# Kernel tuning notes

Hardware: AMD Instinct MI355X
Metric: run time of the kernel (lower is better)

Reference implementation:

```python
import jax, jax.numpy as jnp
import numpy as np

N_NODES = 30000
N_EDGES = 480000
NFEAT = 256
HEADS = 4
C0 = 64      # layer0 out_channels
C1 = 40      # layer1 out_channels = nclass
NEG_SLOPE = 0.2
EPS = 1e-16


def glorot(key, shape, fan):
    # PyG glorot: uniform(-s, s), s = sqrt(6/(fan_in+fan_out)) over last 2 dims
    s = float(np.sqrt(6.0 / fan))
    return jax.random.uniform(key, shape, jnp.float32, -s, s)


def setup_inputs() -> dict:
    key = jax.random.key(0)
    ks = jax.random.split(key, 10)
    x = jax.random.normal(ks[0], (N_NODES, NFEAT), jnp.float32)
    src = jax.random.randint(ks[1], (N_EDGES,), 0, N_NODES)
    off = jax.random.randint(ks[2], (N_EDGES,), 1, N_NODES)
    dst = (src + off) % N_NODES  # guaranteed no self loops
    edge_index = jnp.stack([src, dst]).astype(jnp.int64)
    # layer 0 params (in=256 -> heads*out = 4*64, concat=True)
    w0 = glorot(ks[3], (NFEAT, HEADS * C0), NFEAT + HEADS * C0)
    att0 = glorot(ks[4], (1, HEADS, 2 * C0), HEADS + 2 * C0)
    b0 = jnp.zeros((HEADS * C0,), jnp.float32)
    # layer 1 params (in=256 -> heads*out = 4*40, concat=False)
    w1 = glorot(ks[5], (HEADS * C0, HEADS * C1), HEADS * C0 + HEADS * C1)
    att1 = glorot(ks[6], (1, HEADS, 2 * C1), HEADS + 2 * C1)
    b1 = jnp.zeros((C1,), jnp.float32)
    return {"x": x, "edge_index": edge_index, "w0": w0, "att0": att0,
            "b0": b0, "w1": w1, "att1": att1, "b1": b1}


def geo_layer(x, row, col, W, att, bias, heads, out_ch, concat):
    n = x.shape[0]
    h = (x @ W).reshape(n, heads, out_ch)          # [N,H,C]
    x_i = h[row]                                   # [E,H,C] gather (target per old-PyG i=0)
    x_j = h[col]                                   # [E,H,C]
    # 'gat' attention: leaky_relu(sum(cat(x_i,x_j) * att))
    a_l = att[:, :, :out_ch]
    a_r = att[:, :, out_ch:]
    alpha = jnp.sum(x_i * a_l, -1) + jnp.sum(x_j * a_r, -1)   # [E,H]
    alpha = jax.nn.leaky_relu(alpha, NEG_SLOPE)
    # segment softmax over target node (row)
    amax = jax.ops.segment_max(alpha, row, num_segments=n)
    ex = jnp.exp(alpha - amax[row])
    denom = jax.ops.segment_sum(ex, row, num_segments=n)
    alpha = ex / (denom[row] + EPS)
    neighbor = x_j * alpha[..., None]              # [E,H,C]
    out = jax.ops.segment_sum(neighbor, row, num_segments=n)  # [N,H,C]
    if concat:
        out = out.reshape(n, heads * out_ch)
    else:
        out = out.mean(axis=1)
    return out + bias


def reference(x, edge_index, w0, att0, b0, w1, att1, b1):
    n = x.shape[0]
    loops = jnp.arange(n, dtype=edge_index.dtype)
    row = jnp.concatenate([edge_index[0], loops])
    col = jnp.concatenate([edge_index[1], loops])
    out = geo_layer(x, row, col, w0, att0, b0, HEADS, C0, True)
    out = jax.nn.relu(out)
    out = geo_layer(out, row, col, w1, att1, b1, HEADS, C1, False)
    return out  # [N, nclass]
```

## Files before the change

kernel.cpp:

```cpp
#include <hip/hip_runtime.h>
#include <math.h>

#define N_NODES 30000
#define N_EDGESN 480000
#define NFEAT 256
#define HEADS 4
#define C0V 64
#define C1V 40
#define HC0 (HEADS*C0V)
#define HC1 (HEADS*C1V)
#define NEG_SLOPE 0.2f
#define EPSV 1e-16f
#define KDIM 256
#define KPAD 264

typedef unsigned short ushort_t;
typedef __attribute__((ext_vector_type(8))) short short8v;
typedef __attribute__((ext_vector_type(4))) float f32x4;

__device__ __forceinline__ float lrelu(float x) { return x >= 0.f ? x : x * NEG_SLOPE; }

__device__ __forceinline__ float b2f_lo(unsigned int u) {
  union { unsigned int u; float f; } v; v.u = u << 16; return v.f;
}
__device__ __forceinline__ float b2f_hi(unsigned int u) {
  union { unsigned int u; float f; } v; v.u = u & 0xffff0000u; return v.f;
}
__device__ __forceinline__ unsigned short f2b(float f) {
  union { float f; unsigned int u; } v; v.f = f;
  unsigned int u = v.u + 0x7FFFu + ((v.u >> 16) & 1u);
  return (unsigned short)(u >> 16);
}

__global__ __launch_bounds__(256) void prep_kernel(const float* __restrict__ W0,
    const float* __restrict__ W1, ushort_t* __restrict__ W0t,
    ushort_t* __restrict__ W1t, int* __restrict__ zp, int zn) {
  const int idx = blockIdx.x * 256 + threadIdx.x;
  constexpr int T0 = NFEAT * HC0;
  constexpr int T1 = HC0 * HC1;
  if (idx < T0) {
    const int k = idx / HC0, nf = idx - k * HC0;
    W0t[(size_t)nf * NFEAT + k] = f2b(W0[idx]);
  } else if (idx < T0 + T1) {
    const int i2 = idx - T0;
    const int k = i2 / HC1, nf = i2 - k * HC1;
    W1t[(size_t)nf * HC0 + k] = f2b(W1[i2]);
  }
  if (idx < zn) zp[idx] = 0;
}

template <int NFW, int CG, bool A_F32, int FUSE, int NT>
__global__ __launch_bounds__(NT) void gemm_mfma3(const void* __restrict__ Ap,
    const ushort_t* __restrict__ Wt, ushort_t* __restrict__ C, int nblk,
    const float* __restrict__ att, float* __restrict__ al, float* __restrict__ ar) {
  constexpr int S = N_NODES / 16;
  constexpr int N = CG * NFW * 16;
  constexpr int NCH = 16 * (KDIM / 8) / NT;
  __shared__ ushort_t As[2][16][KPAD];
  const int tid = threadIdx.x;
  const int lane = tid & 63, cg = tid >> 6;
  const int r_a = lane & 15, kg = lane >> 4;

  short8v B[8][NFW];
#pragma unroll
  for (int ks = 0; ks < 8; ++ks)
#pragma unroll
    for (int f = 0; f < NFW; ++f)
      B[ks][f] = *reinterpret_cast<const short8v*>(
          Wt + (size_t)((cg * NFW + f) * 16 + r_a) * KDIM + ks * 32 + kg * 8);

#define STAGE_LOAD(STRIP, STG)                                                   \
  _Pragma("unroll")                                                              \
  for (int q = 0; q < NCH; ++q) {                                                \
    const int c = tid + q * NT;                                                  \
    const int r = c >> 5, ko = (c & 31) * 8;                                     \
    if (A_F32) {                                                                 \
      const float* A = (const float*)Ap + (size_t)((STRIP) * 16 + r) * KDIM + ko;\
      const float4 lo = *reinterpret_cast<const float4*>(A);                     \
      const float4 hi = *reinterpret_cast<const float4*>(A + 4);                 \
      STG[q].x = (unsigned)f2b(lo.x) | ((unsigned)f2b(lo.y) << 16);              \
      STG[q].y = (unsigned)f2b(lo.z) | ((unsigned)f2b(lo.w) << 16);              \
      STG[q].z = (unsigned)f2b(hi.x) | ((unsigned)f2b(hi.y) << 16);              \
      STG[q].w = (unsigned)f2b(hi.z) | ((unsigned)f2b(hi.w) << 16);              \
    } else {                                                                     \
      STG[q] = *reinterpret_cast<const uint4*>(                                  \
          (const ushort_t*)Ap + (size_t)((STRIP) * 16 + r) * KDIM + ko);         \
    }                                                                            \
  }
#define STAGE_WRITE(BUF, STG)                                                    \
  _Pragma("unroll")                                                              \
  for (int q = 0; q < NCH; ++q) {                                                \
    const int c = tid + q * NT;                                                  \
    const int r = c >> 5, ko = (c & 31) * 8;                                     \
    *reinterpret_cast<uint4*>(&As[BUF][r][ko]) = STG[q];                         \
  }

  int strip = blockIdx.x;
  {
    uint4 stg[NCH];
    STAGE_LOAD(strip, stg)
    STAGE_WRITE(0, stg)
  }
  __syncthreads();

  int buf = 0;
  while (true) {
    const int next = strip + nblk;
    const bool has_next = next < S;
    uint4 stg[NCH];
    if (has_next) { STAGE_LOAD(next, stg) }

    f32x4 acc[NFW];
#pragma unroll
    for (int f = 0; f < NFW; ++f) acc[f] = (f32x4){0.f, 0.f, 0.f, 0.f};
#pragma unroll
    for (int ks = 0; ks < 8; ++ks) {
      const short8v a =
          *reinterpret_cast<const short8v*>(&As[buf][r_a][ks * 32 + kg * 8]);
#pragma unroll
      for (int f = 0; f < NFW; ++f)
        acc[f] = __builtin_amdgcn_mfma_f32_16x16x32_bf16(a, B[ks][f], acc[f], 0, 0, 0);
    }
    const int row0 = strip * 16;
#pragma unroll
    for (int f = 0; f < NFW; ++f) {
#pragma unroll
      for (int r = 0; r < 4; ++r) {
        C[(size_t)(row0 + kg * 4 + r) * N + (cg * NFW + f) * 16 + r_a] =
            f2b(acc[f][r]);
      }
    }
    if (FUSE == 1) {
      float hpl[4] = {0.f, 0.f, 0.f, 0.f}, hpr[4] = {0.f, 0.f, 0.f, 0.f};
#pragma unroll
      for (int f = 0; f < NFW; ++f) {
        const int cc = f * 16 + r_a;
        const float wlv = att[cg * 128 + cc];
        const float wrv = att[cg * 128 + 64 + cc];
#pragma unroll
        for (int r = 0; r < 4; ++r) {
          hpl[r] = fmaf(acc[f][r], wlv, hpl[r]);
          hpr[r] = fmaf(acc[f][r], wrv, hpr[r]);
        }
      }
#pragma unroll
      for (int o = 1; o < 16; o <<= 1) {
#pragma unroll
        for (int r = 0; r < 4; ++r) {
          hpl[r] += __shfl_xor(hpl[r], o);
          hpr[r] += __shfl_xor(hpr[r], o);
        }
      }
      if (r_a == 0) {
#pragma unroll
        for (int r = 0; r < 4; ++r) {
          const int row = row0 + kg * 4 + r;
          al[(size_t)row * 4 + cg] = hpl[r];
          ar[(size_t)row * 4 + cg] = hpr[r];
        }
      }
    } else if (FUSE == 2) {
      float hpa[4] = {0,0,0,0}, hpb[4] = {0,0,0,0};
      float hra[4] = {0,0,0,0}, hrb[4] = {0,0,0,0};
#pragma unroll
      for (int f = 0; f < NFW; ++f) {
        const int col = cg * 80 + f * 16 + r_a;
        const int hd = col / 40;
        const int cc = col - hd * 40;
        const float wlv = att[hd * 80 + cc];
        const float wrv = att[hd * 80 + 40 + cc];
        const bool isB = (hd & 1);
#pragma unroll
        for (int r = 0; r < 4; ++r) {
          const float v = acc[f][r];
          if (isB) { hpb[r] = fmaf(v, wlv, hpb[r]); hrb[r] = fmaf(v, wrv, hrb[r]); }
          else     { hpa[r] = fmaf(v, wlv, hpa[r]); hra[r] = fmaf(v, wrv, hra[r]); }
        }
      }
#pragma unroll
      for (int o = 1; o < 16; o <<= 1) {
#pragma unroll
        for (int r = 0; r < 4; ++r) {
          hpa[r] += __shfl_xor(hpa[r], o); hpb[r] += __shfl_xor(hpb[r], o);
          hra[r] += __shfl_xor(hra[r], o); hrb[r] += __shfl_xor(hrb[r], o);
        }
      }
      if (r_a == 0) {
#pragma unroll
        for (int r = 0; r < 4; ++r) {
          const int row = row0 + kg * 4 + r;
          al[(size_t)row * 4 + cg * 2 + 0] = hpa[r];
          al[(size_t)row * 4 + cg * 2 + 1] = hpb[r];
          ar[(size_t)row * 4 + cg * 2 + 0] = hra[r];
          ar[(size_t)row * 4 + cg * 2 + 1] = hrb[r];
        }
      }
    }

    if (!has_next) break;
    STAGE_WRITE(buf ^ 1, stg)
    __syncthreads();
    strip = next; buf ^= 1;
  }
#undef STAGE_LOAD
#undef STAGE_WRITE
}

__global__ void hist_kernel(const int* __restrict__ src, int* __restrict__ deg, int E) {
  const int e = blockIdx.x * blockDim.x + threadIdx.x;
  if (e < E) atomicAdd(&deg[src[e]], 1);
}

__global__ __launch_bounds__(256) void alloc_kernel(const int* __restrict__ deg,
    int* __restrict__ rowstart, int* __restrict__ counter, int n) {
  const int i = blockIdx.x * 256 + threadIdx.x;
  const int lane = threadIdx.x & 63;
  const int d = (i < n) ? deg[i] : 0;
  int x = d;
#pragma unroll
  for (int o = 1; o < 64; o <<= 1) { int y = __shfl_up(x, o); if (lane >= o) x += y; }
  int base = 0;
  if (lane == 63) base = atomicAdd(counter, x);
  base = __shfl(base, 63);
  if (i < n) rowstart[i] = base + x - d;
}

__global__ void scatter_kernel(const int* __restrict__ src, const int* __restrict__ dst,
    const int* __restrict__ rowstart, int* __restrict__ fill, int* __restrict__ scol,
    int E) {
  const int e = blockIdx.x * blockDim.x + threadIdx.x;
  if (e < E) {
    const int r = src[e];
    const int pos = rowstart[r] + atomicAdd(&fill[r], 1);
    scol[pos] = dst[e];
  }
}

template <int C, bool CONCAT_RELU>
__global__ __launch_bounds__(256) void gat_agg6(const ushort_t* __restrict__ h,
    const float* __restrict__ al, const float* __restrict__ ar,
    const int* __restrict__ rowstart, const int* __restrict__ deg,
    const int* __restrict__ scol, const float* __restrict__ bias,
    void* __restrict__ outv, int n) {
  constexpr int ROW = HEADS * C;
  constexpr int LPG = ROW / 8;
  constexpr int NG  = 64 / LPG;
  __shared__ float smA[CONCAT_RELU ? 1 : 4][CONCAT_RELU ? 1 : NG]
                      [CONCAT_RELU ? 1 : ROW];
  __shared__ float smT[CONCAT_RELU ? 1 : 4][CONCAT_RELU ? 1 : NG * LPG];
  const int wid = threadIdx.x >> 6, lane = threadIdx.x & 63;
  const int i = blockIdx.x * 4 + wid;
  if (i >= n) return;
  const int s0 = rowstart[i];
  const int s1 = s0 + deg[i];

  const float4 al4 = *reinterpret_cast<const float4*>(al + (size_t)i * 4);
  const float4 ari = *reinterpret_cast<const float4*>(ar + (size_t)i * 4);
  const float es0 = __expf(lrelu(al4.x + ari.x));
  const float es1 = __expf(lrelu(al4.y + ari.y));
  const float es2 = __expf(lrelu(al4.z + ari.z));
  const float es3 = __expf(lrelu(al4.w + ari.w));

  const int g  = lane / LPG;
  const int cl = lane - g * LPG;
  const bool act = g < NG;
  const int hd = (cl * 8) / C;
  const float al_h = hd < 2 ? (hd == 0 ? al4.x : al4.y) : (hd == 2 ? al4.z : al4.w);
  const float es_h = hd < 2 ? (hd == 0 ? es0 : es1) : (hd == 2 ? es2 : es3);

  float t = 0.f;
  float acc[8];
#pragma unroll
  for (int k = 0; k < 8; ++k) acc[k] = 0.f;

  if (g == 0) {
    const uint4 hv = *reinterpret_cast<const uint4*>(h + (size_t)i * ROW + cl * 8);
    acc[0] = es_h * b2f_lo(hv.x); acc[1] = es_h * b2f_hi(hv.x);
    acc[2] = es_h * b2f_lo(hv.y); acc[3] = es_h * b2f_hi(hv.y);
    acc[4] = es_h * b2f_lo(hv.z); acc[5] = es_h * b2f_hi(hv.z);
    acc[6] = es_h * b2f_lo(hv.w); acc[7] = es_h * b2f_hi(hv.w);
  }

#define FMA8(W, HV) \
  acc[0] = fmaf(W, b2f_lo(HV.x), acc[0]); acc[1] = fmaf(W, b2f_hi(HV.x), acc[1]); \
  acc[2] = fmaf(W, b2f_lo(HV.y), acc[2]); acc[3] = fmaf(W, b2f_hi(HV.y), acc[3]); \
  acc[4] = fmaf(W, b2f_lo(HV.z), acc[4]); acc[5] = fmaf(W, b2f_hi(HV.z), acc[5]); \
  acc[6] = fmaf(W, b2f_lo(HV.w), acc[6]); acc[7] = fmaf(W, b2f_hi(HV.w), acc[7])
#define EDGE1(J) { \
  const float a_ = ar[(size_t)(J) * 4 + hd]; \
  const uint4 hv_ = *reinterpret_cast<const uint4*>(h + (size_t)(J) * ROW + cl * 8); \
  const float w_ = __expf(lrelu(al_h + a_)); \
  t += w_; \
  FMA8(w_, hv_); }

  if (act) {
    int e = s0 + g;
    int j0 = scol[e];
    int j1 = scol[e + NG];
    int j2 = scol[e + 2 * NG];
    int j3 = scol[e + 3 * NG];
    for (; e + 3 * NG < s1; e += 4 * NG) {
      const int p0 = scol[e + 4 * NG];
      const int p1 = scol[e + 5 * NG];
      const int p2 = scol[e + 6 * NG];
      const int p3 = scol[e + 7 * NG];
      const float a0 = ar[(size_t)j0 * 4 + hd];
      const float a1 = ar[(size_t)j1 * 4 + hd];
      const float a2 = ar[(size_t)j2 * 4 + hd];
      const float a3 = ar[(size_t)j3 * 4 + hd];
      const uint4 h0_ = *reinterpret_cast<const uint4*>(h + (size_t)j0 * ROW + cl * 8);
      const uint4 h1_ = *reinterpret_cast<const uint4*>(h + (size_t)j1 * ROW + cl * 8);
      const uint4 h2_ = *reinterpret_cast<const uint4*>(h + (size_t)j2 * ROW + cl * 8);
      const uint4 h3_ = *reinterpret_cast<const uint4*>(h + (size_t)j3 * ROW + cl * 8);
      const float w0 = __expf(lrelu(al_h + a0));
      const float w1 = __expf(lrelu(al_h + a1));
      const float w2 = __expf(lrelu(al_h + a2));
      const float w3 = __expf(lrelu(al_h + a3));
      t += (w0 + w1) + (w2 + w3);
      FMA8(w0, h0_); FMA8(w1, h1_); FMA8(w2, h2_); FMA8(w3, h3_);
      j0 = p0; j1 = p1; j2 = p2; j3 = p3;
    }
    if (e < s1) {
      EDGE1(j0)
      e += NG;
      if (e < s1) {
        EDGE1(j1)
        e += NG;
        if (e < s1) EDGE1(j2)
      }
    }
  }
#undef EDGE1
#undef FMA8

  if (CONCAT_RELU) {
    t += __shfl_xor(t, 32);
    const float inv = 1.f / (t + es_h + EPSV);
#pragma unroll
    for (int k = 0; k < 8; ++k) acc[k] *= inv;
#pragma unroll
    for (int k = 0; k < 8; ++k) acc[k] += __shfl_xor(acc[k], 32);
    if (g == 0) {
      const float4 blo = *reinterpret_cast<const float4*>(bias + cl * 8);
      const float4 bhi = *reinterpret_cast<const float4*>(bias + cl * 8 + 4);
      uint4 st;
      st.x = (unsigned)f2b(fmaxf(acc[0] + blo.x, 0.f)) |
             ((unsigned)f2b(fmaxf(acc[1] + blo.y, 0.f)) << 16);
      st.y = (unsigned)f2b(fmaxf(acc[2] + blo.z, 0.f)) |
             ((unsigned)f2b(fmaxf(acc[3] + blo.w, 0.f)) << 16);
      st.z = (unsigned)f2b(fmaxf(acc[4] + bhi.x, 0.f)) |
             ((unsigned)f2b(fmaxf(acc[5] + bhi.y, 0.f)) << 16);
      st.w = (unsigned)f2b(fmaxf(acc[6] + bhi.z, 0.f)) |
             ((unsigned)f2b(fmaxf(acc[7] + bhi.w, 0.f)) << 16);
      *reinterpret_cast<uint4*>((ushort_t*)outv + (size_t)i * ROW + cl * 8) = st;
    }
  } else {
    if (act) {
#pragma unroll
      for (int k = 0; k < 8; ++k) smA[wid][g][cl * 8 + k] = acc[k];
      smT[wid][g * LPG + cl] = t;
    }
    __syncthreads();
    if (lane < C) {
      const float es[4] = {es0, es1, es2, es3};
      float s = 0.f;
#pragma unroll
      for (int hh = 0; hh < HEADS; ++hh) {
        float den = es[hh];
#pragma unroll
        for (int gg = 0; gg < NG; ++gg)
          den += smT[wid][gg * LPG + hh * 5];
        float chan = 0.f;
#pragma unroll
        for (int gg = 0; gg < NG; ++gg) chan += smA[wid][gg][hh * C + lane];
        s += chan / (den + EPSV);
      }
      ((float*)outv)[(size_t)i * C + lane] = s * 0.25f + bias[lane];
    }
  }
}

extern "C" void kernel_launch(void* const* d_in, const int* in_sizes, int n_in,
                              void* d_out, int out_size, void* d_ws, size_t ws_size,
                              hipStream_t stream) {
  const float* x    = (const float*)d_in[0];
  const int*   ei   = (const int*)d_in[1];
  const float* w0   = (const float*)d_in[2];
  const float* att0 = (const float*)d_in[3];
  const float* b0   = (const float*)d_in[4];
  const float* w1   = (const float*)d_in[5];
  const float* att1 = (const float*)d_in[6];
  const float* b1   = (const float*)d_in[7];
  float* out = (float*)d_out;

  char* ws = (char*)d_ws;
  size_t off = 0;
  auto alloc = [&](size_t bytes) -> void* {
    void* p = ws + off;
    off += (bytes + 255) & ~(size_t)255;
    return p;
  };
  ushort_t* h0b = (ushort_t*)alloc((size_t)N_NODES * HC0 * 2);
  ushort_t* o0b = (ushort_t*)alloc((size_t)N_NODES * HC0 * 2);
  float* al0 = (float*)alloc((size_t)N_NODES * HEADS * 4);
  float* ar0 = (float*)alloc((size_t)N_NODES * HEADS * 4);
  ushort_t* w0t = (ushort_t*)alloc((size_t)HC0 * NFEAT * 2);
  ushort_t* w1t = (ushort_t*)alloc((size_t)HC1 * HC0 * 2);
  int* deg      = (int*)alloc((size_t)N_NODES * 4);
  int* fill     = (int*)alloc((size_t)N_NODES * 4);
  int* counter  = (int*)alloc(256);
  int* rowstart = (int*)alloc((size_t)N_NODES * 4);
  int* scol     = (int*)alloc((size_t)(N_EDGESN + 64) * 4);
  ushort_t* h1b = h0b;
  float* al1 = al0;
  float* ar1 = ar0;

  const int* srcp = ei;
  const int* dstp = ei + N_EDGESN;

  const int ztot = (int)(counter - deg) + 1;
  constexpr int PREPN = NFEAT * HC0 + HC0 * HC1;
  prep_kernel<<<(PREPN + 255) / 256, 256, 0, stream>>>(w0, w1, w0t, w1t, deg, ztot);
  hist_kernel<<<(N_EDGESN + 255) / 256, 256, 0, stream>>>(srcp, deg, N_EDGESN);
  alloc_kernel<<<(N_NODES + 255) / 256, 256, 0, stream>>>(deg, rowstart, counter,
                                                          N_NODES);
  scatter_kernel<<<(N_EDGESN + 255) / 256, 256, 0, stream>>>(srcp, dstp, rowstart,
                                                             fill, scol, N_EDGESN);

  gemm_mfma3<4, 4, true, 1, 256><<<625, 256, 0, stream>>>(
      x, w0t, h0b, 625, att0, al0, ar0);
  gat_agg6<C0V, true><<<(N_NODES + 3) / 4, 256, 0, stream>>>(
      h0b, al0, ar0, rowstart, deg, scol, b0, o0b, N_NODES);
  gemm_mfma3<5, 2, false, 2, 128><<<938, 128, 0, stream>>>(
      o0b, w1t, h1b, 938, att1, al1, ar1);
  gat_agg6<C1V, false><<<(N_NODES + 3) / 4, 256, 0, stream>>>(
      h1b, al1, ar1, rowstart, deg, scol, b1, out, N_NODES);
}
```

Baseline: 172.2 us.

## Merge CSR build and weight prep into one cooperative kernel with grid syncs

Replaces the four separate launches (weight transpose/zeroing, degree histogram, row allocation, edge scatter) with a single cooperative kernel of 1024 blocks that uses grid.sync() between phases. This is meant to remove per-launch overhead and the gaps between the small preprocessing kernels. In exchange it adds grid-wide barrier cost and limits the work to a fixed grid with grid-stride loops, and it depends on the cooperative launch succeeding with 1024 co-resident blocks.

New measurement: 447.4 us. +159.8%, slower.

```diff
diff --git a/kernel.cpp b/kernel.cpp
--- a/kernel.cpp
+++ b/kernel.cpp
@@ -1,5 +1,8 @@
 #include <hip/hip_runtime.h>
+#include <hip/hip_cooperative_groups.h>
 #include <math.h>
+
+namespace cg = cooperative_groups;
 
 #define N_NODES 30000
 #define N_EDGESN 480000
@@ -32,21 +35,49 @@
   return (unsigned short)(u >> 16);
 }
 
-__global__ __launch_bounds__(256) void prep_kernel(const float* __restrict__ W0,
-    const float* __restrict__ W1, ushort_t* __restrict__ W0t,
-    ushort_t* __restrict__ W1t, int* __restrict__ zp, int zn) {
-  const int idx = blockIdx.x * 256 + threadIdx.x;
-  constexpr int T0 = NFEAT * HC0;
-  constexpr int T1 = HC0 * HC1;
-  if (idx < T0) {
+__global__ __launch_bounds__(256) void csr_build(
+    const float* __restrict__ W0, const float* __restrict__ W1,
+    ushort_t* __restrict__ W0t, ushort_t* __restrict__ W1t,
+    const int* __restrict__ src, const int* __restrict__ dst,
+    int* __restrict__ deg, int* __restrict__ fill, int* __restrict__ counter,
+    int* __restrict__ rowstart, int* __restrict__ scol, int ztot) {
+  cg::grid_group grid = cg::this_grid();
+  const int gsz = gridDim.x * 256;
+  const int gtid = blockIdx.x * 256 + threadIdx.x;
+  const int lane = threadIdx.x & 63;
+
+  for (int idx = gtid; idx < NFEAT * HC0; idx += gsz) {
     const int k = idx / HC0, nf = idx - k * HC0;
     W0t[(size_t)nf * NFEAT + k] = f2b(W0[idx]);
-  } else if (idx < T0 + T1) {
-    const int i2 = idx - T0;
-    const int k = i2 / HC1, nf = i2 - k * HC1;
-    W1t[(size_t)nf * HC0 + k] = f2b(W1[i2]);
-  }
-  if (idx < zn) zp[idx] = 0;
+  }
+  for (int idx = gtid; idx < HC0 * HC1; idx += gsz) {
+    const int k = idx / HC1, nf = idx - k * HC1;
+    W1t[(size_t)nf * HC0 + k] = f2b(W1[idx]);
+  }
+  for (int idx = gtid; idx < ztot; idx += gsz) deg[idx] = 0;
+  grid.sync();
+
+  for (int e = gtid; e < N_EDGESN; e += gsz) atomicAdd(&deg[src[e]], 1);
+  grid.sync();
+
+  constexpr int NPAD = (N_NODES + 63) & ~63;
+  for (int i = gtid; i < NPAD; i += gsz) {
+    const int d = (i < N_NODES) ? deg[i] : 0;
+    int x = d;
+#pragma unroll
+    for (int o = 1; o < 64; o <<= 1) { int y = __shfl_up(x, o); if (lane >= o) x += y; }
+    int base = 0;
+    if (lane == 63) base = atomicAdd(counter, x);
+    base = __shfl(base, 63);
+    if (i < N_NODES) rowstart[i] = base + x - d;
+  }
+  grid.sync();
+
+  for (int e = gtid; e < N_EDGESN; e += gsz) {
+    const int r = src[e];
+    const int pos = rowstart[r] + atomicAdd(&fill[r], 1);
+    scol[pos] = dst[e];
+  }
 }
 
 template <int NFW, int CG, bool A_F32, int FUSE, int NT>
@@ -58,7 +89,7 @@
   constexpr int NCH = 16 * (KDIM / 8) / NT;
   __shared__ ushort_t As[2][16][KPAD];
   const int tid = threadIdx.x;
-  const int lane = tid & 63, cg = tid >> 6;
+  const int lane = tid & 63, cg_ = tid >> 6;
   const int r_a = lane & 15, kg = lane >> 4;
 
   short8v B[8][NFW];
@@ -67,7 +98,7 @@
 #pragma unroll
     for (int f = 0; f < NFW; ++f)
       B[ks][f] = *reinterpret_cast<const short8v*>(
-          Wt + (size_t)((cg * NFW + f) * 16 + r_a) * KDIM + ks * 32 + kg * 8);
+          Wt + (size_t)((cg_ * NFW + f) * 16 + r_a) * KDIM + ks * 32 + kg * 8);
 
 #define STAGE_LOAD(STRIP, STG)                                                   \
   _Pragma("unroll")                                                              \
@@ -126,7 +157,7 @@
     for (int f = 0; f < NFW; ++f) {
 #pragma unroll
       for (int r = 0; r < 4; ++r) {
-        C[(size_t)(row0 + kg * 4 + r) * N + (cg * NFW + f) * 16 + r_a] =
+        C[(size_t)(row0 + kg * 4 + r) * N + (cg_ * NFW + f) * 16 + r_a] =
             f2b(acc[f][r]);
       }
     }
@@ -135,8 +166,8 @@
 #pragma unroll
       for (int f = 0; f < NFW; ++f) {
         const int cc = f * 16 + r_a;
-        const float wlv = att[cg * 128 + cc];
-        const float wrv = att[cg * 128 + 64 + cc];
+        const float wlv = att[cg_ * 128 + cc];
+        const float wrv = att[cg_ * 128 + 64 + cc];
 #pragma unroll
         for (int r = 0; r < 4; ++r) {
           hpl[r] = fmaf(acc[f][r], wlv, hpl[r]);
@@ -155,8 +186,8 @@
 #pragma unroll
         for (int r = 0; r < 4; ++r) {
           const int row = row0 + kg * 4 + r;
-          al[(size_t)row * 4 + cg] = hpl[r];
-          ar[(size_t)row * 4 + cg] = hpr[r];
+          al[(size_t)row * 4 + cg_] = hpl[r];
+          ar[(size_t)row * 4 + cg_] = hpr[r];
         }
       }
     } else if (FUSE == 2) {
@@ -164,7 +195,7 @@
       float hra[4] = {0,0,0,0}, hrb[4] = {0,0,0,0};
 #pragma unroll
       for (int f = 0; f < NFW; ++f) {
-        const int col = cg * 80 + f * 16 + r_a;
+        const int col = cg_ * 80 + f * 16 + r_a;
         const int hd = col / 40;
         const int cc = col - hd * 40;
         const float wlv = att[hd * 80 + cc];
@@ -189,10 +220,10 @@
 #pragma unroll
         for (int r = 0; r < 4; ++r) {
           const int row = row0 + kg * 4 + r;
-          al[(size_t)row * 4 + cg * 2 + 0] = hpa[r];
-          al[(size_t)row * 4 + cg * 2 + 1] = hpb[r];
-          ar[(size_t)row * 4 + cg * 2 + 0] = hra[r];
-          ar[(size_t)row * 4 + cg * 2 + 1] = hrb[r];
+          al[(size_t)row * 4 + cg_ * 2 + 0] = hpa[r];
+          al[(size_t)row * 4 + cg_ * 2 + 1] = hpb[r];
+          ar[(size_t)row * 4 + cg_ * 2 + 0] = hra[r];
+          ar[(size_t)row * 4 + cg_ * 2 + 1] = hrb[r];
         }
       }
     }
@@ -204,36 +235,6 @@
   }
 #undef STAGE_LOAD
 #undef STAGE_WRITE
-}
-
-__global__ void hist_kernel(const int* __restrict__ src, int* __restrict__ deg, int E) {
-  const int e = blockIdx.x * blockDim.x + threadIdx.x;
-  if (e < E) atomicAdd(&deg[src[e]], 1);
-}
-
-__global__ __launch_bounds__(256) void alloc_kernel(const int* __restrict__ deg,
-    int* __restrict__ rowstart, int* __restrict__ counter, int n) {
-  const int i = blockIdx.x * 256 + threadIdx.x;
-  const int lane = threadIdx.x & 63;
-  const int d = (i < n) ? deg[i] : 0;
-  int x = d;
-#pragma unroll
-  for (int o = 1; o < 64; o <<= 1) { int y = __shfl_up(x, o); if (lane >= o) x += y; }
-  int base = 0;
-  if (lane == 63) base = atomicAdd(counter, x);
-  base = __shfl(base, 63);
-  if (i < n) rowstart[i] = base + x - d;
-}
-
-__global__ void scatter_kernel(const int* __restrict__ src, const int* __restrict__ dst,
-    const int* __restrict__ rowstart, int* __restrict__ fill, int* __restrict__ scol,
-    int E) {
-  const int e = blockIdx.x * blockDim.x + threadIdx.x;
-  if (e < E) {
-    const int r = src[e];
-    const int pos = rowstart[r] + atomicAdd(&fill[r], 1);
-    scol[pos] = dst[e];
-  }
 }
 
 template <int C, bool CONCAT_RELU>
@@ -418,14 +419,16 @@
   const int* srcp = ei;
   const int* dstp = ei + N_EDGESN;
 
-  const int ztot = (int)(counter - deg) + 1;
-  constexpr int PREPN = NFEAT * HC0 + HC0 * HC1;
-  prep_kernel<<<(PREPN + 255) / 256, 256, 0, stream>>>(w0, w1, w0t, w1t, deg, ztot);
-  hist_kernel<<<(N_EDGESN + 255) / 256, 256, 0, stream>>>(srcp, deg, N_EDGESN);
-  alloc_kernel<<<(N_NODES + 255) / 256, 256, 0, stream>>>(deg, rowstart, counter,
-                                                          N_NODES);
-  scatter_kernel<<<(N_EDGESN + 255) / 256, 256, 0, stream>>>(srcp, dstp, rowstart,
-                                                             fill, scol, N_EDGESN);
+  int ztot = (int)(counter - deg) + 1;
+
+  {
+    void* args[] = {(void*)&w0, (void*)&w1, (void*)&w0t, (void*)&w1t,
+                    (void*)&srcp, (void*)&dstp, (void*)&deg, (void*)&fill,
+                    (void*)&counter, (void*)&rowstart, (void*)&scol,
+                    (void*)&ztot};
+    hipLaunchCooperativeKernel((void*)csr_build, dim3(1024), dim3(256), args, 0,
+                               stream);
+  }
 
   gemm_mfma3<4, 4, true, 1, 256><<<625, 256, 0, stream>>>(
       x, w0t, h0b, 625, att0, al0, ar0);
```
